# Kernel tuning notes

Measured on AMD Instinct MI355X. Metric: run time of the kernel, lower is better.

The kernel has to match this reference:

```python
import jax, jax.numpy as jnp
import numpy as np

N_CLASSES = 64  # number of initial (labeled) classes


def _compute_logits_radii(h, protos, radii):
    """Complex-valued radii logits.
    h: [B,N,2,D] (real/imag), protos: [B,2,C,D], radii: [B,C].
    dist[b,n,c] = sum_d (hr-pr)^2 + (hi-pi)^2 (matches _compute_distances_complex).
    logits = -dist / (2*radii)  (standard IMP radii-logit form).
    Expanded as |h|^2 + |p|^2 - 2 h.p so the cross term is a GEMM (no [N,C,D] tensor).
    """
    hr, hi = h[:, :, 0, :], h[:, :, 1, :]          # [B,N,D]
    pr, pi = protos[:, 0], protos[:, 1]            # [B,C,D]
    h_sq = jnp.sum(hr * hr + hi * hi, axis=-1)     # [B,N]
    p_sq = jnp.sum(pr * pr + pi * pi, axis=-1)     # [B,C]
    cross = jnp.einsum('bnd,bcd->bnc', hr, pr) + jnp.einsum('bnd,bcd->bnc', hi, pi)
    dist = h_sq[:, :, None] + p_sq[:, None, :] - 2.0 * cross   # [B,N,C]
    return -dist / (2.0 * radii[:, None, :])


def setup_inputs() -> dict:
    key = jax.random.key(0)
    k1, k2, k3, k4, k5 = jax.random.split(key, 5)
    B, N, C, D = 1, 8192, 512, 512
    h = jax.random.normal(k1, (B, N, 2, D), dtype=jnp.float32)
    protos = jax.random.normal(k2, (B, 2, C, D), dtype=jnp.float32)
    # radii must be positive (it divides the distance); keep away from 0
    radii = jax.random.uniform(k3, (B, C), dtype=jnp.float32) * 0.9 + 0.1
    y = jax.random.randint(k4, (N,), 0, N_CLASSES)
    support_labels = jax.random.randint(k5, (C,), 0, N_CLASSES)
    return {"h": h, "protos": protos, "radii": radii, "y": y,
            "support_labels": support_labels, "n_initial_clusters": N_CLASSES}


def reference(h, protos, radii, y, support_labels, n_initial_clusters):
    logits = _compute_logits_radii(h, protos, radii)[0]          # [N,C], B=1 squeeze
    labels = jnp.where(y >= n_initial_clusters, -1, y)           # [N]
    support_targets = labels[:, None] == support_labels[None, :]  # [N,C] bool

    neg_inf = jnp.asarray(-jnp.inf, logits.dtype)
    # best prototype among the query's own class ('or' target)
    target_logits = jnp.where(support_targets, logits, neg_inf)
    best_targets = jnp.argmax(target_logits, axis=1)             # [N]

    # vectorized per-class best prototype: weights[n,c]=1 iff c is the argmax
    # of logits[n,:] restricted to clusters whose label == support_labels[c]
    max_per_class = jax.ops.segment_max(logits.T, support_labels,
                                        num_segments=N_CLASSES)  # [K,N]
    weights = (logits == max_per_class[support_labels, :].T).astype(logits.dtype)  # [N,C]

    # weighted cross entropy at the 'or' target
    log_probs = jax.nn.log_softmax(logits, axis=1)
    nll = -jnp.take_along_axis(log_probs, best_targets[:, None], axis=1)[:, 0]
    w = jnp.take_along_axis(weights, best_targets[:, None], axis=1)[:, 0]
    loss = jnp.mean(nll * w)

    # accuracy: predicted cluster -> its class label
    support_preds = jnp.argmax(logits, axis=1)
    y_pred = support_labels[support_preds]
    acc_val = jnp.sum((y_pred == labels).astype(jnp.float32))
    return loss, acc_val
```

## Files before the change

kernel.cpp:

```cpp
#include <hip/hip_runtime.h>
#include <stdint.h>

typedef unsigned short u16;
typedef __attribute__((ext_vector_type(8))) short shortx8;
typedef __attribute__((ext_vector_type(4))) float floatx4;

#define N_ROWS 8192
#define N_COLS 512
#define KDIM   1024

__device__ __forceinline__ u16 f2bf(float f) {
    union { float f; uint32_t u; } x; x.f = f;
    uint32_t u = x.u;
    uint32_t r = (u + 0x7FFFu + ((u >> 16) & 1u)) >> 16;
    return (u16)r;
}

__device__ __forceinline__ void async_copy16(const void* g, void* l) {
    __builtin_amdgcn_global_load_lds(
        (const __attribute__((address_space(1))) void*)g,
        (__attribute__((address_space(3))) void*)l, 16, 0, 0);
}

__global__ __launch_bounds__(256) void conv_hp(const float* __restrict__ h,
                                               const float* __restrict__ protos,
                                               u16* __restrict__ hb,
                                               u16* __restrict__ bb,
                                               float* __restrict__ hsq,
                                               float* __restrict__ psq) {
    int t = threadIdx.x, lane = t & 63, w = t >> 6;
    int bid = blockIdx.x;
    if (bid < 512) {
        int wave = bid * 4 + w;
        for (int q = 0; q < 4; q++) {
            int row = wave * 4 + q;
            const float4* src = (const float4*)(h + (size_t)row * KDIM);
            ushort4* dst = (ushort4*)(hb + (size_t)row * KDIM);
            float s = 0.0f;
            #pragma unroll
            for (int j = 0; j < 4; j++) {
                float4 v = src[lane + j * 64];
                s += v.x * v.x + v.y * v.y + v.z * v.z + v.w * v.w;
                dst[lane + j * 64] = make_ushort4(f2bf(v.x), f2bf(v.y), f2bf(v.z), f2bf(v.w));
            }
            #pragma unroll
            for (int off = 32; off; off >>= 1) s += __shfl_xor(s, off);
            if (lane == 0) hsq[row] = s;
        }
    } else {
        int c = (bid - 512) * 4 + w;
        const float4* pr = (const float4*)(protos + (size_t)c * 512);
        const float4* pi = (const float4*)(protos + 512 * 512 + (size_t)c * 512);
        ushort4* dr = (ushort4*)(bb + (size_t)c * KDIM);
        ushort4* di = (ushort4*)(bb + (size_t)c * KDIM + 512);
        float s = 0.0f;
        #pragma unroll
        for (int j = 0; j < 2; j++) {
            float4 a = pr[lane + j * 64];
            float4 b = pi[lane + j * 64];
            s += a.x * a.x + a.y * a.y + a.z * a.z + a.w * a.w;
            s += b.x * b.x + b.y * b.y + b.z * b.z + b.w * b.w;
            dr[lane + j * 64] = make_ushort4(f2bf(a.x), f2bf(a.y), f2bf(a.z), f2bf(a.w));
            di[lane + j * 64] = make_ushort4(f2bf(b.x), f2bf(b.y), f2bf(b.z), f2bf(b.w));
        }
        #pragma unroll
        for (int off = 32; off; off >>= 1) s += __shfl_xor(s, off);
        if (lane == 0) psq[c] = s;
    }
}

__global__ __launch_bounds__(256) void gemm_logits(const u16* __restrict__ hb,
                                                   const u16* __restrict__ bb,
                                                   const float* __restrict__ hsq,
                                                   const float* __restrict__ psq,
                                                   const float* __restrict__ radii,
                                                   float* __restrict__ logits) {
    constexpr int BM = 128, BN = 64, BK = 64;
    __shared__ __align__(16) u16 As[BM * BK];
    __shared__ __align__(16) u16 Bs[BN * BK];

    int t = threadIdx.x, lane = t & 63, w = t >> 6;
    int wr = (w & 1) * 64;
    int wc = (w >> 1) * 32;
    int bm0 = blockIdx.x * BM;
    int bn0 = blockIdx.y * BN;

    int tr = t >> 3, tc = t & 7;
    const u16* gA[4]; u16* lA[4];
    #pragma unroll
    for (int i = 0; i < 4; i++) {
        int row = tr + 32 * i;
        int kc = tc ^ (row & 7);
        gA[i] = hb + (size_t)(bm0 + row) * KDIM + kc * 8;
        lA[i] = &As[(t + 256 * i) * 8];
    }
    const u16* gB[2]; u16* lB[2];
    #pragma unroll
    for (int i = 0; i < 2; i++) {
        int row = tr + 32 * i;
        int kc = tc ^ (row & 7);
        gB[i] = bb + (size_t)(bn0 + row) * KDIM + kc * 8;
        lB[i] = &Bs[(t + 256 * i) * 8];
    }

    floatx4 acc[4][2] = {};

    int kq = lane >> 4, l7 = lane & 7, m = lane & 15;
    int swz0 = ((kq) ^ l7) * 8;
    int swz1 = ((4 + kq) ^ l7) * 8;
    const u16* paA = &As[(wr + m) * BK];
    const u16* paB = &Bs[(wc + m) * BK];

    for (int k0 = 0; k0 < KDIM; k0 += BK) {
        __syncthreads();
        #pragma unroll
        for (int i = 0; i < 4; i++) async_copy16(gA[i], lA[i]);
        #pragma unroll
        for (int i = 0; i < 2; i++) async_copy16(gB[i], lB[i]);
        #pragma unroll
        for (int i = 0; i < 4; i++) gA[i] += BK;
        #pragma unroll
        for (int i = 0; i < 2; i++) gB[i] += BK;
        __syncthreads();

        #pragma unroll
        for (int s = 0; s < 2; s++) {
            int sw = s ? swz1 : swz0;
            shortx8 af[4], bf[2];
            #pragma unroll
            for (int i = 0; i < 4; i++) af[i] = *(const shortx8*)(paA + i * 16 * BK + sw);
            #pragma unroll
            for (int j = 0; j < 2; j++) bf[j] = *(const shortx8*)(paB + j * 16 * BK + sw);
            #pragma unroll
            for (int i = 0; i < 4; i++)
                #pragma unroll
                for (int j = 0; j < 2; j++)
                    acc[i][j] = __builtin_amdgcn_mfma_f32_16x16x32_bf16(af[i], bf[j], acc[i][j], 0, 0, 0);
        }
    }

    #pragma unroll
    for (int j = 0; j < 2; j++) {
        int c = bn0 + wc + j * 16 + m;
        float ps = psq[c];
        float inv = 0.5f / radii[c];
        #pragma unroll
        for (int i = 0; i < 4; i++) {
            int rbase = bm0 + wr + i * 16 + kq * 4;
            #pragma unroll
            for (int r = 0; r < 4; r++) {
                int n = rbase + r;
                logits[(size_t)n * N_COLS + c] = (2.0f * acc[i][j][r] - hsq[n] - ps) * inv;
            }
        }
    }
}

__global__ __launch_bounds__(256) void row_reduce(const float* __restrict__ logits,
                                                  const int* __restrict__ y,
                                                  const int* __restrict__ slab,
                                                  const int* __restrict__ ninit_p,
                                                  float* __restrict__ out) {
    int t = threadIdx.x, lane = t & 63, w = t >> 6;
    int wave = blockIdx.x * 4 + w;
    int ninit = ninit_p[0];
    int slab0 = slab[0];

    int s8[8];
    #pragma unroll
    for (int k = 0; k < 8; k++) s8[k] = slab[lane * 8 + k];

    float loss_acc = 0.0f, acc_acc = 0.0f;

    for (int q = 0; q < 4; q++) {
        int row = wave * 4 + q;
        int yv = y[row];
        int lab = (yv >= ninit) ? -1 : yv;
        const float4* lr = (const float4*)(logits + (size_t)row * N_COLS);
        float4 v0 = lr[lane * 2], v1 = lr[lane * 2 + 1];
        float l[8] = {v0.x, v0.y, v0.z, v0.w, v1.x, v1.y, v1.z, v1.w};

        float gmax = -INFINITY; int gidx = 0x7fffffff;
        float rmax = -INFINITY; int ridx = 0x7fffffff;
        float c0max = -INFINITY;
        #pragma unroll
        for (int k = 0; k < 8; k++) {
            int c = lane * 8 + k;
            float v = l[k];
            if (v > gmax) { gmax = v; gidx = c; }
            if (s8[k] == lab && v > rmax) { rmax = v; ridx = c; }
            if (s8[k] == slab0 && v > c0max) c0max = v;
        }
        #pragma unroll
        for (int off = 32; off; off >>= 1) {
            float ov = __shfl_xor(gmax, off); int oi = __shfl_xor(gidx, off);
            if (ov > gmax || (ov == gmax && oi < gidx)) { gmax = ov; gidx = oi; }
            float orv = __shfl_xor(rmax, off); int ori = __shfl_xor(ridx, off);
            if (orv > rmax || (orv == rmax && ori < ridx)) { rmax = orv; ridx = ori; }
            float oc = __shfl_xor(c0max, off);
            if (oc > c0max) c0max = oc;
        }
        float s = 0.0f;
        #pragma unroll
        for (int k = 0; k < 8; k++) s += __expf(l[k] - gmax);
        #pragma unroll
        for (int off = 32; off; off >>= 1) s += __shfl_xor(s, off);

        int ypred = slab[gidx];
        if (lane == 0) {
            float lse = gmax + __logf(s);
            float nll, wgt;
            if (ridx != 0x7fffffff) {
                nll = lse - rmax; wgt = 1.0f;
            } else {
                float l0 = l[0];
                nll = lse - l0;
                wgt = (l0 == c0max) ? 1.0f : 0.0f;
            }
            loss_acc += nll * wgt;
            acc_acc  += (ypred == lab) ? 1.0f : 0.0f;
        }
    }

    __shared__ float pl[4], pa_[4];
    if (lane == 0) { pl[w] = loss_acc * (1.0f / (float)N_ROWS); pa_[w] = acc_acc; }
    __syncthreads();
    if (t == 0) {
        atomicAdd(&out[0], pl[0] + pl[1] + pl[2] + pl[3]);
        atomicAdd(&out[1], pa_[0] + pa_[1] + pa_[2] + pa_[3]);
    }
}

extern "C" void kernel_launch(void* const* d_in, const int* in_sizes, int n_in,
                              void* d_out, int out_size, void* d_ws, size_t ws_size,
                              hipStream_t stream) {
    const float* h      = (const float*)d_in[0];
    const float* protos = (const float*)d_in[1];
    const float* radii  = (const float*)d_in[2];
    const int*   y      = (const int*)d_in[3];
    const int*   slab   = (const int*)d_in[4];
    const int*   ninit  = (const int*)d_in[5];
    float* out = (float*)d_out;

    char* ws = (char*)d_ws;
    u16*   hb     = (u16*)(ws);
    u16*   bb     = (u16*)(ws + 16777216);
    float* hsq    = (float*)(ws + 17825792);
    float* psq    = (float*)(ws + 17858560);
    float* logits = (float*)(ws + 17860608);

    hipMemsetAsync(d_out, 0, 2 * sizeof(float), stream);

    conv_hp<<<640, 256, 0, stream>>>(h, protos, hb, bb, hsq, psq);
    dim3 g(N_ROWS / 128, N_COLS / 64);
    gemm_logits<<<g, 256, 0, stream>>>(hb, bb, hsq, psq, radii, logits);
    row_reduce<<<512, 256, 0, stream>>>(logits, y, slab, ninit, out);
}
```

Baseline: 125.8 us.

## Fuse row reductions into GEMM epilogue with per-tile partials and combine pass

The GEMM epilogue no longer writes the full 8192x512 fp32 logits matrix. Each tile computes per-row partial max/argmax, class-restricted max, class-0 max and a rescaled exp-sum using shuffles and shared memory. A small combine kernel merges the 8 column-block partials per row into loss and accuracy. This removes about 16 MB of logits write and read traffic, at the cost of extra epilogue work (exp, shuffles, y loads per row) and another sync in the GEMM.

```diff
diff --git a/kernel.cpp b/kernel.cpp
--- a/kernel.cpp
+++ b/kernel.cpp
@@ -69,15 +69,28 @@
     }
 }
 
-__global__ __launch_bounds__(256) void gemm_logits(const u16* __restrict__ hb,
-                                                   const u16* __restrict__ bb,
-                                                   const float* __restrict__ hsq,
-                                                   const float* __restrict__ psq,
-                                                   const float* __restrict__ radii,
-                                                   float* __restrict__ logits) {
+__global__ __launch_bounds__(256) void gemm_partials(const u16* __restrict__ hb,
+                                                     const u16* __restrict__ bb,
+                                                     const float* __restrict__ hsq,
+                                                     const float* __restrict__ psq,
+                                                     const float* __restrict__ radii,
+                                                     const int* __restrict__ y,
+                                                     const int* __restrict__ slab,
+                                                     const int* __restrict__ ninit_p,
+                                                     float* __restrict__ pmax_g,
+                                                     int* __restrict__ pidx_g,
+                                                     float* __restrict__ prmax_g,
+                                                     float* __restrict__ pc0_g,
+                                                     float* __restrict__ psum_g,
+                                                     float* __restrict__ l0arr) {
     constexpr int BM = 128, BN = 64, BK = 64;
     __shared__ __align__(16) u16 As[BM * BK];
     __shared__ __align__(16) u16 Bs[BN * BK];
+    __shared__ float smax[2][128];
+    __shared__ int   scol[2][128];
+    __shared__ float srmx[2][128];
+    __shared__ float sc0v[2][128];
+    __shared__ float ssum[2][128];
 
     int t = threadIdx.x, lane = t & 63, w = t >> 6;
     int wr = (w & 1) * 64;
@@ -139,91 +152,120 @@
         }
     }
 
-    #pragma unroll
-    for (int j = 0; j < 2; j++) {
-        int c = bn0 + wc + j * 16 + m;
-        float ps = psq[c];
-        float inv = 0.5f / radii[c];
-        #pragma unroll
-        for (int i = 0; i < 4; i++) {
-            int rbase = bm0 + wr + i * 16 + kq * 4;
-            #pragma unroll
-            for (int r = 0; r < 4; r++) {
-                int n = rbase + r;
-                logits[(size_t)n * N_COLS + c] = (2.0f * acc[i][j][r] - hsq[n] - ps) * inv;
+    int c0 = bn0 + wc + m, c1 = c0 + 16;
+    float ps0 = psq[c0], ps1 = psq[c1];
+    float inv0 = 0.5f / radii[c0], inv1 = 0.5f / radii[c1];
+    int sl0 = slab[c0], sl1 = slab[c1];
+    int slabz = slab[0];
+    int ninit = ninit_p[0];
+    int ch = w >> 1;
+    bool isL0 = (bn0 == 0) && (wc == 0) && (m == 0);
+
+    #pragma unroll
+    for (int i = 0; i < 4; i++) {
+        #pragma unroll
+        for (int r = 0; r < 4; r++) {
+            int n = bm0 + wr + i * 16 + kq * 4 + r;
+            float hsqn = hsq[n];
+            int yv = y[n];
+            int lab = (yv >= ninit) ? -1 : yv;
+            float v0 = (2.0f * acc[i][0][r] - hsqn - ps0) * inv0;
+            float v1 = (2.0f * acc[i][1][r] - hsqn - ps1) * inv1;
+            if (isL0) l0arr[n] = v0;
+
+            float bmax = v0; int bcol = c0;
+            if (v1 > bmax) { bmax = v1; bcol = c1; }
+            float brm = -INFINITY;
+            if (sl0 == lab) brm = v0;
+            if (sl1 == lab && v1 > brm) brm = v1;
+            float bc0 = -INFINITY;
+            if (sl0 == slabz) bc0 = v0;
+            if (sl1 == slabz && v1 > bc0) bc0 = v1;
+            #pragma unroll
+            for (int off = 1; off < 16; off <<= 1) {
+                float ov = __shfl_xor(bmax, off); int oc = __shfl_xor(bcol, off);
+                if (ov > bmax || (ov == bmax && oc < bcol)) { bmax = ov; bcol = oc; }
+                float orv = __shfl_xor(brm, off); if (orv > brm) brm = orv;
+                float oc0 = __shfl_xor(bc0, off); if (oc0 > bc0) bc0 = oc0;
+            }
+            float se = __expf(v0 - bmax) + __expf(v1 - bmax);
+            #pragma unroll
+            for (int off = 1; off < 16; off <<= 1) se += __shfl_xor(se, off);
+            if (m == 0) {
+                int rl = (w & 1) * 64 + i * 16 + kq * 4 + r;
+                smax[ch][rl] = bmax; scol[ch][rl] = bcol;
+                srmx[ch][rl] = brm;  sc0v[ch][rl] = bc0; ssum[ch][rl] = se;
             }
         }
     }
-}
-
-__global__ __launch_bounds__(256) void row_reduce(const float* __restrict__ logits,
-                                                  const int* __restrict__ y,
-                                                  const int* __restrict__ slab,
-                                                  const int* __restrict__ ninit_p,
-                                                  float* __restrict__ out) {
+    __syncthreads();
+    if (t < 128) {
+        int n = bm0 + t;
+        size_t gi_ = (size_t)blockIdx.y * N_ROWS + n;
+        float m0 = smax[0][t], m1 = smax[1][t];
+        int i0 = scol[0][t], i1 = scol[1][t];
+        float gm; int gi;
+        if (m0 > m1 || (m0 == m1 && i0 < i1)) { gm = m0; gi = i0; }
+        else { gm = m1; gi = i1; }
+        pmax_g[gi_] = gm;
+        pidx_g[gi_] = gi;
+        prmax_g[gi_] = fmaxf(srmx[0][t], srmx[1][t]);
+        pc0_g[gi_]  = fmaxf(sc0v[0][t], sc0v[1][t]);
+        psum_g[gi_] = ssum[0][t] * __expf(m0 - gm) + ssum[1][t] * __expf(m1 - gm);
+    }
+}
+
+__global__ __launch_bounds__(256) void combine(const float* __restrict__ pmax_g,
+                                               const int* __restrict__ pidx_g,
+                                               const float* __restrict__ prmax_g,
+                                               const float* __restrict__ pc0_g,
+                                               const float* __restrict__ psum_g,
+                                               const float* __restrict__ l0arr,
+                                               const int* __restrict__ y,
+                                               const int* __restrict__ slab,
+                                               const int* __restrict__ ninit_p,
+                                               float* __restrict__ out) {
     int t = threadIdx.x, lane = t & 63, w = t >> 6;
-    int wave = blockIdx.x * 4 + w;
-    int ninit = ninit_p[0];
-    int slab0 = slab[0];
-
-    int s8[8];
-    #pragma unroll
-    for (int k = 0; k < 8; k++) s8[k] = slab[lane * 8 + k];
-
-    float loss_acc = 0.0f, acc_acc = 0.0f;
-
-    for (int q = 0; q < 4; q++) {
-        int row = wave * 4 + q;
-        int yv = y[row];
-        int lab = (yv >= ninit) ? -1 : yv;
-        const float4* lr = (const float4*)(logits + (size_t)row * N_COLS);
-        float4 v0 = lr[lane * 2], v1 = lr[lane * 2 + 1];
-        float l[8] = {v0.x, v0.y, v0.z, v0.w, v1.x, v1.y, v1.z, v1.w};
-
-        float gmax = -INFINITY; int gidx = 0x7fffffff;
-        float rmax = -INFINITY; int ridx = 0x7fffffff;
-        float c0max = -INFINITY;
-        #pragma unroll
-        for (int k = 0; k < 8; k++) {
-            int c = lane * 8 + k;
-            float v = l[k];
-            if (v > gmax) { gmax = v; gidx = c; }
-            if (s8[k] == lab && v > rmax) { rmax = v; ridx = c; }
-            if (s8[k] == slab0 && v > c0max) c0max = v;
-        }
-        #pragma unroll
-        for (int off = 32; off; off >>= 1) {
-            float ov = __shfl_xor(gmax, off); int oi = __shfl_xor(gidx, off);
-            if (ov > gmax || (ov == gmax && oi < gidx)) { gmax = ov; gidx = oi; }
-            float orv = __shfl_xor(rmax, off); int ori = __shfl_xor(ridx, off);
-            if (orv > rmax || (orv == rmax && ori < ridx)) { rmax = orv; ridx = ori; }
-            float oc = __shfl_xor(c0max, off);
-            if (oc > c0max) c0max = oc;
-        }
-        float s = 0.0f;
-        #pragma unroll
-        for (int k = 0; k < 8; k++) s += __expf(l[k] - gmax);
-        #pragma unroll
-        for (int off = 32; off; off >>= 1) s += __shfl_xor(s, off);
-
-        int ypred = slab[gidx];
-        if (lane == 0) {
-            float lse = gmax + __logf(s);
-            float nll, wgt;
-            if (ridx != 0x7fffffff) {
-                nll = lse - rmax; wgt = 1.0f;
-            } else {
-                float l0 = l[0];
-                nll = lse - l0;
-                wgt = (l0 == c0max) ? 1.0f : 0.0f;
-            }
-            loss_acc += nll * wgt;
-            acc_acc  += (ypred == lab) ? 1.0f : 0.0f;
-        }
-    }
-
+    int n = blockIdx.x * 256 + t;
+
+    float gm = -INFINITY; int gi = 0x7fffffff;
+    float rm = -INFINITY, c0m = -INFINITY;
+    float pm[8];
+    #pragma unroll
+    for (int cb = 0; cb < 8; cb++) {
+        size_t idx = (size_t)cb * N_ROWS + n;
+        float p = pmax_g[idx]; int pi = pidx_g[idx];
+        pm[cb] = p;
+        if (p > gm || (p == gm && pi < gi)) { gm = p; gi = pi; }
+        rm = fmaxf(rm, prmax_g[idx]);
+        c0m = fmaxf(c0m, pc0_g[idx]);
+    }
+    float den = 0.0f;
+    #pragma unroll
+    for (int cb = 0; cb < 8; cb++)
+        den += psum_g[(size_t)cb * N_ROWS + n] * __expf(pm[cb] - gm);
+    float lse = gm + __logf(den);
+
+    int yv = y[n];
+    int lab = (yv >= ninit_p[0]) ? -1 : yv;
+    float nll, wgt;
+    if (rm != -INFINITY) { nll = lse - rm; wgt = 1.0f; }
+    else {
+        float l0 = l0arr[n];
+        nll = lse - l0;
+        wgt = (l0 == c0m) ? 1.0f : 0.0f;
+    }
+    int ypred = slab[gi];
+    float li = nll * wgt * (1.0f / (float)N_ROWS);
+    float ai = (ypred == lab) ? 1.0f : 0.0f;
+
+    #pragma unroll
+    for (int off = 32; off; off >>= 1) {
+        li += __shfl_xor(li, off);
+        ai += __shfl_xor(ai, off);
+    }
     __shared__ float pl[4], pa_[4];
-    if (lane == 0) { pl[w] = loss_acc * (1.0f / (float)N_ROWS); pa_[w] = acc_acc; }
+    if (lane == 0) { pl[w] = li; pa_[w] = ai; }
     __syncthreads();
     if (t == 0) {
         atomicAdd(&out[0], pl[0] + pl[1] + pl[2] + pl[3]);
@@ -243,16 +285,23 @@
     float* out = (float*)d_out;
 
     char* ws = (char*)d_ws;
-    u16*   hb     = (u16*)(ws);
-    u16*   bb     = (u16*)(ws + 16777216);
-    float* hsq    = (float*)(ws + 17825792);
-    float* psq    = (float*)(ws + 17858560);
-    float* logits = (float*)(ws + 17860608);
+    u16*   hb    = (u16*)(ws);
+    u16*   bb    = (u16*)(ws + 16777216);
+    float* hsq   = (float*)(ws + 17825792);
+    float* psq   = (float*)(ws + 17858560);
+    float* pmax  = (float*)(ws + 17860608);
+    int*   pidx  = (int*)  (ws + 18122752);
+    float* prmax = (float*)(ws + 18384896);
+    float* pc0   = (float*)(ws + 18647040);
+    float* psum  = (float*)(ws + 18909184);
+    float* l0arr = (float*)(ws + 19171328);
 
     hipMemsetAsync(d_out, 0, 2 * sizeof(float), stream);
 
     conv_hp<<<640, 256, 0, stream>>>(h, protos, hb, bb, hsq, psq);
     dim3 g(N_ROWS / 128, N_COLS / 64);
-    gemm_logits<<<g, 256, 0, stream>>>(hb, bb, hsq, psq, radii, logits);
-    row_reduce<<<512, 256, 0, stream>>>(logits, y, slab, ninit, out);
-}
+    gemm_partials<<<g, 256, 0, stream>>>(hb, bb, hsq, psq, radii, y, slab, ninit,
+                                         pmax, pidx, prmax, pc0, psum, l0arr);
+    combine<<<N_ROWS / 256, 256, 0, stream>>>(pmax, pidx, prmax, pc0, psum,
+                                              l0arr, y, slab, ninit, out);
+}
```

New measurement: 117.4 us. -6.7%, faster.
